# Kernel tuning notes

Hardware: AMD Instinct MI355X
Metric: run time of the kernel (lower is better)

## Reference

```python
import jax, jax.numpy as jnp
import numpy as np

N, E, H, B, L = 100000, 600000, 128, 512, 10


def setup_inputs() -> dict:
    key = jax.random.key(0)
    ks = jax.random.split(key, 16)
    def lin(k, fan_in, fan_out):
        return (jax.random.normal(k, (fan_in, fan_out), jnp.float32) / np.sqrt(fan_in)).astype(jnp.float32)
    inp = {
        'node_reps_0': jax.random.normal(ks[0], (N, H), jnp.float32),
        'node_reps_1': jax.random.normal(ks[1], (N, H), jnp.float32),
        'W1': lin(ks[2], 2 * H, 4 * H), 'b1': jnp.zeros((4 * H,), jnp.float32),
        'W2': lin(ks[3], 4 * H, 2 * H), 'b2': jnp.zeros((2 * H,), jnp.float32),
        'W3': lin(ks[4], 2 * H, H),     'b3': jnp.zeros((H,), jnp.float32),
        'W4': lin(ks[5], H, H),         'b4': jnp.zeros((H,), jnp.float32),
        'W5': lin(ks[6], H, L),         'b5': jnp.zeros((L,), jnp.float32),
        'edge_index': jax.random.randint(ks[7], (2, E), 0, N, jnp.int64 if jax.config.jax_enable_x64 else jnp.int32),
        'batch': jnp.sort(jax.random.randint(ks[8], (N,), 0, B)),
        'y': jax.random.randint(ks[9], (B,), 0, L),
    }
    return inp


def reference(node_reps_0, node_reps_1, W1, b1, W2, b2, W3, b3, W4, b4, W5, b5,
              edge_index, batch, y):
    # ava_node_reps = reps(full graph) - reps(occupied subgraph)
    reps = node_reps_0 - node_reps_1                      # [N, H]
    src, dst = edge_index[0], edge_index[1]               # [E]
    # gather endpoints, concat -> edge action rep MLP (ELU)
    a = jnp.concatenate([reps[src], reps[dst]], axis=1)   # [E, 2H]
    h = jax.nn.elu(a @ W1 + b1)                           # [E, 4H]
    h = jax.nn.elu(h @ W2 + b2)                           # [E, 2H]
    h = h @ W3 + b3                                       # [E, H]
    # edge action prob generator: h -> h -> num_labels
    logits = jax.nn.elu(h @ W4 + b4) @ W5 + b5            # [E, L]
    edge_batch = batch[src]                               # [E] graph id per edge
    target_y = y[edge_batch]                              # [E]
    scores = jnp.take_along_axis(logits, target_y[:, None], axis=1)[:, 0]  # [E]
    # segment-wise (per-graph) softmax over available edges
    seg_max = jax.ops.segment_max(scores, edge_batch, num_segments=B)
    ex = jnp.exp(scores - seg_max[edge_batch])
    seg_sum = jax.ops.segment_sum(ex, edge_batch, num_segments=B)
    probs = ex / seg_sum[edge_batch]                      # [E]
    # scatter_max: per-graph max prob and its (first) argmax edge index
    added_probs = jax.ops.segment_max(probs, edge_batch, num_segments=B)  # [B]
    idx = jnp.arange(E, dtype=edge_batch.dtype)
    cand = jnp.where(probs == added_probs[edge_batch], idx, E)
    added_actions = jax.ops.segment_min(cand, edge_batch, num_segments=B)  # [B]
    return probs, added_probs, added_actions
```

## Files before the change

kernel.cpp:

```cpp
#include <hip/hip_runtime.h>
#include <hip/hip_bf16.h>
#include <cmath>

#define NN 100000
#define EE 600000
#define BB 512
#define LL 10

typedef __attribute__((ext_vector_type(8))) short  bf16x8;
typedef __attribute__((ext_vector_type(4))) float  f32x4;
typedef unsigned int uint;
typedef unsigned short ushort;

__device__ __forceinline__ float elu_f(float x){ return x > 0.f ? x : __expf(x) - 1.f; }

__device__ __forceinline__ ushort bf16_rne(float f){
  uint u = __float_as_uint(f);
  return (ushort)((u + 0x7FFFu + ((u >> 16) & 1u)) >> 16);
}

__device__ __forceinline__ f32x4 MFMA(bf16x8 a, bf16x8 b, f32x4 c){
  return __builtin_amdgcn_mfma_f32_16x16x32_bf16(a, b, c, 0, 0, 0);
}

__device__ __forceinline__ unsigned enc_f(float f){
  unsigned u = __float_as_uint(f);
  return (u & 0x80000000u) ? ~u : (u | 0x80000000u);
}
__device__ __forceinline__ float dec_f(unsigned u){
  return (u & 0x80000000u) ? __uint_as_float(u ^ 0x80000000u) : __uint_as_float(~u);
}
#define ENC_NEG_INF 0x007FFFFFu

#define AROW 260

__global__ __launch_bounds__(256) void kReps(const float* __restrict__ r0,
                                             const float* __restrict__ r1,
                                             ushort* __restrict__ repsF){
  int gid = blockIdx.x*256 + threadIdx.x;
  int n = gid >> 4, k8 = gid & 15;
  const float4* a = (const float4*)(r0 + (size_t)n*128 + k8*8);
  const float4* b = (const float4*)(r1 + (size_t)n*128 + k8*8);
  float4 x0 = a[0], x1 = a[1], y0 = b[0], y1 = b[1];
  float d[8] = {x0.x-y0.x, x0.y-y0.y, x0.z-y0.z, x0.w-y0.w,
                x1.x-y1.x, x1.y-y1.y, x1.z-y1.z, x1.w-y1.w};
  ushort hi[8], lo[8];
  #pragma unroll
  for (int j=0;j<8;++j){
    hi[j] = bf16_rne(d[j]);
    float fh = __uint_as_float(((uint)hi[j])<<16);
    lo[j] = bf16_rne(d[j] - fh);
  }
  ushort* dh = repsF + (size_t)n*256 + k8*8;
  ushort* dl = dh + 128;
  #pragma unroll
  for (int j=0;j<8;++j){ dh[j] = hi[j]; dl[j] = lo[j]; }
}

__global__ __launch_bounds__(256) void kPrepW(const float* __restrict__ W, int N,
                                              int KT, int NT, ushort* __restrict__ dst){
  int gid = blockIdx.x*256 + threadIdx.x;
  int total = KT*NT*64;
  if (gid >= total) return;
  int l = gid & 63, tile = gid >> 6;
  int kt = tile / NT, nt = tile % NT;
  int kbase = kt*32 + (l>>4)*8;
  int n = nt*16 + (l&15);
  int partStride = KT*NT*512;
  int base = tile*512 + l*8;
  #pragma unroll
  for (int j=0;j<8;++j){
    float f = W[(size_t)(kbase+j)*N + n];
    ushort h = bf16_rne(f);
    float fh = __uint_as_float(((uint)h)<<16);
    dst[base + j] = h;
    dst[partStride + base + j] = bf16_rne(f - fh);
  }
}

template<int NTILES>
__device__ __forceinline__ void xposeN(ushort* sT, const f32x4* Cg,
                                       const float* __restrict__ biasPtr,
                                       bool doElu, int l){
  const int quad = l >> 4, r16 = l & 15;
  uint* ldsu = (uint*)sT;
  #pragma unroll
  for (int i = 0; i < NTILES; ++i){
    float bv = biasPtr[i*16 + r16];
    #pragma unroll
    for (int mtl = 0; mtl < 2; ++mtl){
      f32x4 v = Cg[i*2 + mtl];
      ushort hi[4], lo[4];
      #pragma unroll
      for (int r = 0; r < 4; ++r){
        float f = v[r] + bv;
        if (doElu) f = elu_f(f);
        hi[r] = bf16_rne(f);
        float fh = __uint_as_float(((uint)hi[r]) << 16);
        lo[r] = bf16_rne(f - fh);
      }
      uint v01h = (uint)hi[0] | ((uint)hi[1]<<16);
      uint v23h = (uint)hi[2] | ((uint)hi[3]<<16);
      uint v01l = (uint)lo[0] | ((uint)lo[1]<<16);
      uint v23l = (uint)lo[2] | ((uint)lo[3]<<16);
      uint t01h = __shfl_xor(v01h,1), t23h = __shfl_xor(v23h,1);
      uint t01l = __shfl_xor(v01l,1), t23l = __shfl_xor(v23l,1);
      int c2 = (i*16 + (r16 & ~1)) >> 1;
      int m0 = mtl*16 + quad*4;
      if (!(l & 1)){
        ldsu[(m0+0)*34 + c2]        = (v01h & 0xFFFFu) | (t01h << 16);
        ldsu[(m0+1)*34 + c2]        = (v01h >> 16) | (t01h & 0xFFFF0000u);
        ldsu[1088 + (m0+0)*34 + c2] = (v01l & 0xFFFFu) | (t01l << 16);
        ldsu[1088 + (m0+1)*34 + c2] = (v01l >> 16) | (t01l & 0xFFFF0000u);
      } else {
        ldsu[(m0+2)*34 + c2]        = (t23h & 0xFFFFu) | (v23h << 16);
        ldsu[(m0+3)*34 + c2]        = (t23h >> 16) | (v23h & 0xFFFF0000u);
        ldsu[1088 + (m0+2)*34 + c2] = (t23l & 0xFFFFu) | (v23l << 16);
        ldsu[1088 + (m0+3)*34 + c2] = (t23l >> 16) | (v23l & 0xFFFF0000u);
      }
    }
  }
}

__device__ __forceinline__ bf16x8 readA(const ushort* region, int part, int m, int colBase){
  union { uint2 u[2]; bf16x8 v; } cvt;
  const ushort* p = region + part*2176 + m*68 + colBase;
  cvt.u[0] = *(const uint2*)p;
  cvt.u[1] = *(const uint2*)(p + 4);
  return cvt.v;
}

__device__ __forceinline__ bf16x8 loadA8(const ushort* p){
  union { uint2 u[2]; bf16x8 v; } cvt;
  cvt.u[0] = *(const uint2*)p;
  cvt.u[1] = *(const uint2*)(p + 4);
  return cvt.v;
}

__device__ __forceinline__ void produceSlice(int s, int w, int l, int quad, int r16,
    const ushort* sA,
    const ushort* __restrict__ W1F, const float* __restrict__ b1,
    ushort* buf){
  f32x4 C1[2];
  C1[0] = (f32x4)0.f; C1[1] = (f32x4)0.f;
  #pragma unroll
  for (int hk = 0; hk < 8; ++hk){
    const int rbase = (hk < 4) ? 0 : 32;
    const int ko = (hk & 3)*32 + quad*8;
    const ushort* r0p = sA + (rbase + r16)*AROW + ko;
    const ushort* r1p = sA + (rbase + 16 + r16)*AROW + ko;
    bf16x8 Ah0 = loadA8(r0p);
    bf16x8 Al0 = loadA8(r0p + 128);
    bf16x8 Ah1 = loadA8(r1p);
    bf16x8 Al1 = loadA8(r1p + 128);
    const bf16x8* WfH = (const bf16x8*)W1F + ((size_t)hk*32 + s*4 + w)*64 + l;
    const bf16x8* WfL = WfH + 8*32*64;
    bf16x8 Bh = WfH[0], Bl = WfL[0];
    C1[0] = MFMA(Ah0, Bh, C1[0]); C1[1] = MFMA(Ah1, Bh, C1[1]);
    C1[0] = MFMA(Ah0, Bl, C1[0]); C1[1] = MFMA(Ah1, Bl, C1[1]);
    C1[0] = MFMA(Al0, Bh, C1[0]); C1[1] = MFMA(Al1, Bh, C1[1]);
  }
  xposeN<1>(buf + w*16, C1, b1 + s*64 + w*16, true, l);
}

__device__ __forceinline__ void consumeSlice(int s, int w, int l, int quad, int r16,
    const ushort* buf, const ushort* __restrict__ W2F, f32x4 (&C2q)[8]){
  #pragma unroll
  for (int j2 = 0; j2 < 2; ++j2){
    int colBase = j2*32 + quad*8;
    bf16x8 Ah[2], Al[2];
    #pragma unroll
    for (int mtl = 0; mtl < 2; ++mtl){
      int m = mtl*16 + r16;
      Ah[mtl] = readA(buf, 0, m, colBase);
      Al[mtl] = readA(buf, 1, m, colBase);
    }
    const int kt = s*2 + j2;
    const bf16x8* WfH = (const bf16x8*)W2F + ((size_t)kt*16 + w*4)*64 + l;
    const bf16x8* WfL = WfH + 16*16*64;
    #pragma unroll
    for (int j = 0; j < 4; ++j){
      bf16x8 Bh = WfH[j*64], Bl = WfL[j*64];
      f32x4 c0 = C2q[j*2], c1 = C2q[j*2+1];
      c0 = MFMA(Ah[0], Bh, c0); c1 = MFMA(Ah[1], Bh, c1);
      c0 = MFMA(Ah[0], Bl, c0); c1 = MFMA(Ah[1], Bl, c1);
      c0 = MFMA(Al[0], Bh, c0); c1 = MFMA(Al[1], Bh, c1);
      C2q[j*2] = c0; C2q[j*2+1] = c1;
    }
  }
}

__global__ __launch_bounds__(256, 4) void kMLP(
    const ushort* __restrict__ repsF,
    const ushort* __restrict__ W1F, const ushort* __restrict__ W2F,
    const ushort* __restrict__ W3F, const ushort* __restrict__ W4F,
    const float* __restrict__ b1, const float* __restrict__ b2,
    const float* __restrict__ b3, const float* __restrict__ b4,
    const float* __restrict__ W5, const float* __restrict__ b5,
    const int* __restrict__ edge_index, const int* __restrict__ batch,
    const int* __restrict__ y,
    float* __restrict__ scores, int* __restrict__ ebatch)
{
  __shared__ __align__(16) ushort sReg01[2*4352];
  __shared__ __align__(16) ushort sA[64*AROW];
  __shared__ int sTy[32];
  __shared__ int sNode[64];
  __shared__ float sRed[4][32];

  const int tid = threadIdx.x;
  const int w = tid >> 6;
  const int l = tid & 63;
  const int quad = l >> 4, r16 = l & 15;
  const int e0 = blockIdx.x * 32;

  if (tid < 32){
    int s = edge_index[e0 + tid];
    int d = edge_index[EE + e0 + tid];
    sNode[tid] = s;
    sNode[32 + tid] = d;
    int eb = batch[s];
    ebatch[e0 + tid] = eb;
    sTy[tid] = y[eb];
  }
  __syncthreads();

  #pragma unroll
  for (int k = 0; k < 8; ++k){
    int c = tid + k*256;
    int row = c >> 5, col = c & 31;
    const ushort* src = repsF + (size_t)sNode[row]*256 + col*8;
    uint4 v = *(const uint4*)src;
    ushort* dst = sA + row*AROW + col*8;
    *(uint2*)dst        = make_uint2(v.x, v.y);
    *(uint2*)(dst + 4)  = make_uint2(v.z, v.w);
  }
  __syncthreads();

  f32x4 C2q[8];
  #pragma unroll
  for (int i=0;i<8;++i) C2q[i] = (f32x4)0.f;

  produceSlice(0, w, l, quad, r16, sA, W1F, b1, sReg01);
  __syncthreads();
  #pragma unroll 1
  for (int s = 0; s < 8; ++s){
    if (s < 7)
      produceSlice(s+1, w, l, quad, r16, sA, W1F, b1, sReg01 + ((s+1)&1)*4352);
    consumeSlice(s, w, l, quad, r16, sReg01 + (s&1)*4352, W2F, C2q);
    __syncthreads();
  }

  ushort* regW = (w < 2) ? (sReg01 + w*4352) : (sA + (w-2)*4352);
  xposeN<4>(regW, C2q, b2 + w*64, true, l);
  __syncthreads();

  f32x4 C3q[4];
  #pragma unroll
  for (int i=0;i<4;++i) C3q[i] = (f32x4)0.f;
  #pragma unroll
  for (int kt = 0; kt < 8; ++kt){
    int rw = kt >> 1;
    const ushort* reg = (rw < 2) ? (sReg01 + rw*4352) : (sA + (rw-2)*4352);
    int colBase = (kt & 1)*32 + quad*8;
    bf16x8 Ah[2], Al[2];
    #pragma unroll
    for (int mtl = 0; mtl < 2; ++mtl){
      int m = mtl*16 + r16;
      Ah[mtl] = readA(reg, 0, m, colBase);
      Al[mtl] = readA(reg, 1, m, colBase);
    }
    const bf16x8* WfH = (const bf16x8*)W3F + ((size_t)kt*8 + w*2)*64 + l;
    const bf16x8* WfL = WfH + 8*8*64;
    #pragma unroll
    for (int j = 0; j < 2; ++j){
      bf16x8 Bh = WfH[j*64], Bl = WfL[j*64];
      f32x4 c0 = C3q[j*2], c1 = C3q[j*2+1];
      c0 = MFMA(Ah[0], Bh, c0); c1 = MFMA(Ah[1], Bh, c1);
      c0 = MFMA(Ah[0], Bl, c0); c1 = MFMA(Ah[1], Bl, c1);
      c0 = MFMA(Al[0], Bh, c0); c1 = MFMA(Al[1], Bh, c1);
      C3q[j*2] = c0; C3q[j*2+1] = c1;
    }
  }
  __syncthreads();

  xposeN<2>(sReg01 + (w>>1)*4352 + (w&1)*32, C3q, b3 + w*32, false, l);
  __syncthreads();

  f32x4 C4q[4];
  #pragma unroll
  for (int i=0;i<4;++i) C4q[i] = (f32x4)0.f;
  #pragma unroll
  for (int kt = 0; kt < 4; ++kt){
    const ushort* reg = sReg01 + (kt>>1)*4352;
    int colBase = (kt & 1)*32 + quad*8;
    bf16x8 Ah[2], Al[2];
    #pragma unroll
    for (int mtl = 0; mtl < 2; ++mtl){
      int m = mtl*16 + r16;
      Ah[mtl] = readA(reg, 0, m, colBase);
      Al[mtl] = readA(reg, 1, m, colBase);
    }
    const bf16x8* WfH = (const bf16x8*)W4F + ((size_t)kt*8 + w*2)*64 + l;
    const bf16x8* WfL = WfH + 4*8*64;
    #pragma unroll
    for (int j = 0; j < 2; ++j){
      bf16x8 Bh = WfH[j*64], Bl = WfL[j*64];
      f32x4 c0 = C4q[j*2], c1 = C4q[j*2+1];
      c0 = MFMA(Ah[0], Bh, c0); c1 = MFMA(Ah[1], Bh, c1);
      c0 = MFMA(Ah[0], Bl, c0); c1 = MFMA(Ah[1], Bl, c1);
      c0 = MFMA(Al[0], Bh, c0); c1 = MFMA(Al[1], Bh, c1);
      C4q[j*2] = c0; C4q[j*2+1] = c1;
    }
  }

  int tvals[2][4];
  #pragma unroll
  for (int mtl=0;mtl<2;++mtl)
    #pragma unroll
    for (int r=0;r<4;++r) tvals[mtl][r] = sTy[mtl*16 + quad*4 + r];

  float p[2][4] = {{0.f,0.f,0.f,0.f},{0.f,0.f,0.f,0.f}};
  #pragma unroll
  for (int j = 0; j < 2; ++j){
    int n4 = (w*2 + j)*16 + r16;
    float bv = b4[n4];
    const float* w5r = W5 + n4*LL;
    #pragma unroll
    for (int mtl = 0; mtl < 2; ++mtl){
      f32x4 c = C4q[j*2+mtl];
      #pragma unroll
      for (int r=0;r<4;++r)
        p[mtl][r] += elu_f(c[r] + bv) * w5r[tvals[mtl][r]];
    }
  }
  #pragma unroll
  for (int d = 8; d >= 1; d >>= 1){
    #pragma unroll
    for (int mtl=0;mtl<2;++mtl)
      #pragma unroll
      for (int r=0;r<4;++r)
        p[mtl][r] += __shfl_down(p[mtl][r], d, 16);
  }
  if (r16 == 0){
    #pragma unroll
    for (int mtl=0;mtl<2;++mtl)
      #pragma unroll
      for (int r=0;r<4;++r){
        int m = mtl*16 + quad*4 + r;
        sRed[w][m] = p[mtl][r];
      }
  }
  __syncthreads();
  if (tid < 32){
    float s = sRed[0][tid] + sRed[1][tid] + sRed[2][tid] + sRed[3][tid];
    scores[e0 + tid] = s + b5[sTy[tid]];
  }
}

__global__ void kInitSeg(unsigned* segmax, float* segsum, unsigned* gmax, int* gact){
  int b = blockIdx.x*blockDim.x + threadIdx.x;
  if (b < BB){ segmax[b] = ENC_NEG_INF; segsum[b] = 0.f; gmax[b] = ENC_NEG_INF; gact[b] = 0x7FFFFFFF; }
}

__global__ __launch_bounds__(256) void kSegMax(const float* __restrict__ scores,
                                               const int* __restrict__ eb,
                                               unsigned* __restrict__ segmax){
  __shared__ unsigned l[BB];
  for (int b = threadIdx.x; b < BB; b += 256) l[b] = 0u;
  __syncthreads();
  for (int e = blockIdx.x*256 + threadIdx.x; e < EE; e += gridDim.x*256)
    atomicMax(&l[eb[e]], enc_f(scores[e]));
  __syncthreads();
  for (int b = threadIdx.x; b < BB; b += 256)
    if (l[b]) atomicMax(&segmax[b], l[b]);
}

__global__ __launch_bounds__(256) void kExpSum(const float* __restrict__ scores,
                                               const int* __restrict__ eb,
                                               const unsigned* __restrict__ segmax,
                                               float* __restrict__ segsum,
                                               float* __restrict__ outprobs){
  __shared__ float l[BB];
  for (int b = threadIdx.x; b < BB; b += 256) l[b] = 0.f;
  __syncthreads();
  for (int e = blockIdx.x*256 + threadIdx.x; e < EE; e += gridDim.x*256){
    int b = eb[e];
    float ex = expf(scores[e] - dec_f(segmax[b]));
    outprobs[e] = ex;
    atomicAdd(&l[b], ex);
  }
  __syncthreads();
  for (int b = threadIdx.x; b < BB; b += 256)
    if (l[b] != 0.f) atomicAdd(&segsum[b], l[b]);
}

__global__ __launch_bounds__(256) void kProbMax(float* __restrict__ outprobs,
                                                const int* __restrict__ eb,
                                                const float* __restrict__ segsum,
                                                unsigned* __restrict__ gmax){
  __shared__ unsigned l[BB];
  for (int b = threadIdx.x; b < BB; b += 256) l[b] = 0u;
  __syncthreads();
  for (int e = blockIdx.x*256 + threadIdx.x; e < EE; e += gridDim.x*256){
    int b = eb[e];
    float p = outprobs[e] / segsum[b];
    outprobs[e] = p;
    atomicMax(&l[b], enc_f(p));
  }
  __syncthreads();
  for (int b = threadIdx.x; b < BB; b += 256)
    if (l[b]) atomicMax(&gmax[b], l[b]);
}

__global__ __launch_bounds__(256) void kArgMin(const float* __restrict__ outprobs,
                                               const int* __restrict__ eb,
                                               const unsigned* __restrict__ gmax,
                                               int* __restrict__ gact){
  __shared__ int l[BB];
  for (int b = threadIdx.x; b < BB; b += 256) l[b] = 0x7FFFFFFF;
  __syncthreads();
  for (int e = blockIdx.x*256 + threadIdx.x; e < EE; e += gridDim.x*256){
    int b = eb[e];
    if (enc_f(outprobs[e]) == gmax[b]) atomicMin(&l[b], e);
  }
  __syncthreads();
  for (int b = threadIdx.x; b < BB; b += 256)
    if (l[b] != 0x7FFFFFFF) atomicMin(&gact[b], l[b]);
}

__global__ void kFinal(const unsigned* __restrict__ gmax, const int* __restrict__ gact,
                       float* __restrict__ out){
  int b = threadIdx.x;
  if (b < BB){
    out[EE + b]      = dec_f(gmax[b]);
    out[EE + BB + b] = (float)gact[b];
  }
}

extern "C" void kernel_launch(void* const* d_in, const int* in_sizes, int n_in,
                              void* d_out, int out_size, void* d_ws, size_t ws_size,
                              hipStream_t stream){
  const float* r0 = (const float*)d_in[0];
  const float* r1 = (const float*)d_in[1];
  const float* W1 = (const float*)d_in[2];
  const float* b1 = (const float*)d_in[3];
  const float* W2 = (const float*)d_in[4];
  const float* b2 = (const float*)d_in[5];
  const float* W3 = (const float*)d_in[6];
  const float* b3 = (const float*)d_in[7];
  const float* W4 = (const float*)d_in[8];
  const float* b4 = (const float*)d_in[9];
  const float* W5 = (const float*)d_in[10];
  const float* b5 = (const float*)d_in[11];
  const int* edge_index = (const int*)d_in[12];
  const int* batch = (const int*)d_in[13];
  const int* y = (const int*)d_in[14];
  float* out = (float*)d_out;

  char* ws = (char*)d_ws;
  size_t off = 0;
  float*    scores = (float*)(ws + off);    off += (size_t)EE*4;
  int*      ebatch = (int*)(ws + off);      off += (size_t)EE*4;
  unsigned* segmax = (unsigned*)(ws + off); off += BB*4;
  float*    segsum = (float*)(ws + off);    off += BB*4;
  unsigned* gmax   = (unsigned*)(ws + off); off += BB*4;
  int*      gact   = (int*)(ws + off);      off += BB*4;
  off = (off + 511) & ~(size_t)511;
  ushort* repsF = (ushort*)(ws + off);      off += (size_t)NN*256*2;
  ushort* W1F   = (ushort*)(ws + off);      off += (size_t)2*8*32*512*2;
  ushort* W2F   = (ushort*)(ws + off);      off += (size_t)2*16*16*512*2;
  ushort* W3F   = (ushort*)(ws + off);      off += (size_t)2*8*8*512*2;
  ushort* W4F   = (ushort*)(ws + off);      off += (size_t)2*4*8*512*2;

  kInitSeg<<<2, 256, 0, stream>>>(segmax, segsum, gmax, gact);
  kReps<<<(NN*16)/256, 256, 0, stream>>>(r0, r1, repsF);
  kPrepW<<<(8*32*64)/256, 256, 0, stream>>>(W1, 512, 8, 32, W1F);
  kPrepW<<<(16*16*64)/256, 256, 0, stream>>>(W2, 256, 16, 16, W2F);
  kPrepW<<<(8*8*64)/256, 256, 0, stream>>>(W3, 128, 8, 8, W3F);
  kPrepW<<<(4*8*64)/256, 256, 0, stream>>>(W4, 128, 4, 8, W4F);

  kMLP<<<EE/32, 256, 0, stream>>>(repsF, W1F, W2F, W3F, W4F,
                                  b1, b2, b3, b4, W5, b5,
                                  edge_index, batch, y, scores, ebatch);

  kSegMax <<<256, 256, 0, stream>>>(scores, ebatch, segmax);
  kExpSum <<<256, 256, 0, stream>>>(scores, ebatch, segmax, segsum, out);
  kProbMax<<<256, 256, 0, stream>>>(out, ebatch, segsum, gmax);
  kArgMin <<<256, 256, 0, stream>>>(out, ebatch, gmax, gact);
  kFinal  <<<1, 512, 0, stream>>>(gmax, gact, out);
}
```

Before: 1.430 ms.

## Split layer-1 gather into src/dst halves to shrink shared memory

Layer 1 now runs in two phases. The src-node rows are gathered into a half-size sA, and the first-half K contributions for all 8 output slices go into register accumulators (C1s[8][2]). The dst rows are then loaded into the same buffer and the second half is finished inside the pipelined produce/consume loop. This cuts the shared-memory footprint so more blocks can reside per CU, but it holds 64 extra accumulator floats per thread and fully unrolls the loop, which risks register pressure or spills under the 256x4 launch bounds.

```diff
diff --git a/kernel.cpp b/kernel.cpp
--- a/kernel.cpp
+++ b/kernel.cpp
@@ -137,30 +137,26 @@
   return cvt.v;
 }
 
-__device__ __forceinline__ void produceSlice(int s, int w, int l, int quad, int r16,
-    const ushort* sA,
-    const ushort* __restrict__ W1F, const float* __restrict__ b1,
-    ushort* buf){
-  f32x4 C1[2];
-  C1[0] = (f32x4)0.f; C1[1] = (f32x4)0.f;
-  #pragma unroll
-  for (int hk = 0; hk < 8; ++hk){
-    const int rbase = (hk < 4) ? 0 : 32;
-    const int ko = (hk & 3)*32 + quad*8;
-    const ushort* r0p = sA + (rbase + r16)*AROW + ko;
-    const ushort* r1p = sA + (rbase + 16 + r16)*AROW + ko;
+__device__ __forceinline__ void produceHalf(int sl, int w, int l, int quad, int r16,
+    const ushort* sA, int hkBase,
+    const ushort* __restrict__ W1F, f32x4 (&C1)[2]){
+  #pragma unroll
+  for (int hh = 0; hh < 4; ++hh){
+    const int hk = hkBase + hh;
+    const int ko = hh*32 + quad*8;
+    const ushort* r0p = sA + r16*AROW + ko;
+    const ushort* r1p = sA + (16 + r16)*AROW + ko;
     bf16x8 Ah0 = loadA8(r0p);
     bf16x8 Al0 = loadA8(r0p + 128);
     bf16x8 Ah1 = loadA8(r1p);
     bf16x8 Al1 = loadA8(r1p + 128);
-    const bf16x8* WfH = (const bf16x8*)W1F + ((size_t)hk*32 + s*4 + w)*64 + l;
+    const bf16x8* WfH = (const bf16x8*)W1F + ((size_t)hk*32 + sl*4 + w)*64 + l;
     const bf16x8* WfL = WfH + 8*32*64;
     bf16x8 Bh = WfH[0], Bl = WfL[0];
     C1[0] = MFMA(Ah0, Bh, C1[0]); C1[1] = MFMA(Ah1, Bh, C1[1]);
     C1[0] = MFMA(Ah0, Bl, C1[0]); C1[1] = MFMA(Ah1, Bl, C1[1]);
     C1[0] = MFMA(Al0, Bh, C1[0]); C1[1] = MFMA(Al1, Bh, C1[1]);
   }
-  xposeN<1>(buf + w*16, C1, b1 + s*64 + w*16, true, l);
 }
 
 __device__ __forceinline__ void consumeSlice(int s, int w, int l, int quad, int r16,
@@ -202,7 +198,7 @@
     float* __restrict__ scores, int* __restrict__ ebatch)
 {
   __shared__ __align__(16) ushort sReg01[2*4352];
-  __shared__ __align__(16) ushort sA[64*AROW];
+  __shared__ __align__(16) ushort sA[2*4352];
   __shared__ int sTy[32];
   __shared__ int sNode[64];
   __shared__ float sRed[4][32];
@@ -225,7 +221,7 @@
   __syncthreads();
 
   #pragma unroll
-  for (int k = 0; k < 8; ++k){
+  for (int k = 0; k < 4; ++k){
     int c = tid + k*256;
     int row = c >> 5, col = c & 31;
     const ushort* src = repsF + (size_t)sNode[row]*256 + col*8;
@@ -236,19 +232,44 @@
   }
   __syncthreads();
 
+  f32x4 C1s[8][2];
+  #pragma unroll
+  for (int s=0;s<8;++s){ C1s[s][0] = (f32x4)0.f; C1s[s][1] = (f32x4)0.f; }
+  #pragma unroll
+  for (int s = 0; s < 8; ++s)
+    produceHalf(s, w, l, quad, r16, sA, 0, W1F, C1s[s]);
+
+  __syncthreads();
+
+  #pragma unroll
+  for (int k = 0; k < 4; ++k){
+    int c = tid + k*256;
+    int row = c >> 5, col = c & 31;
+    const ushort* src = repsF + (size_t)sNode[32 + row]*256 + col*8;
+    uint4 v = *(const uint4*)src;
+    ushort* dst = sA + row*AROW + col*8;
+    *(uint2*)dst        = make_uint2(v.x, v.y);
+    *(uint2*)(dst + 4)  = make_uint2(v.z, v.w);
+  }
+  __syncthreads();
+
   f32x4 C2q[8];
   #pragma unroll
   for (int i=0;i<8;++i) C2q[i] = (f32x4)0.f;
 
-  produceSlice(0, w, l, quad, r16, sA, W1F, b1, sReg01);
-  __syncthreads();
-  #pragma unroll 1
-  for (int s = 0; s < 8; ++s){
-    if (s < 7)
-      produceSlice(s+1, w, l, quad, r16, sA, W1F, b1, sReg01 + ((s+1)&1)*4352);
+  produceHalf(0, w, l, quad, r16, sA, 4, W1F, C1s[0]);
+  xposeN<1>(sReg01 + w*16, C1s[0], b1 + w*16, true, l);
+  __syncthreads();
+  #pragma unroll
+  for (int s = 0; s < 7; ++s){
+    produceHalf(s+1, w, l, quad, r16, sA, 4, W1F, C1s[s+1]);
+    xposeN<1>(sReg01 + ((s+1)&1)*4352 + w*16, C1s[s+1],
+              b1 + (s+1)*64 + w*16, true, l);
     consumeSlice(s, w, l, quad, r16, sReg01 + (s&1)*4352, W2F, C2q);
     __syncthreads();
   }
+  consumeSlice(7, w, l, quad, r16, sReg01 + 4352, W2F, C2q);
+  __syncthreads();
 
   ushort* regW = (w < 2) ? (sReg01 + w*4352) : (sA + (w-2)*4352);
   xposeN<4>(regW, C2q, b2 + w*64, true, l);
```

After: 1.666 ms. 16.5% more time.

## Fuse prob-max and argmin into one packed 64-bit atomicMin pass; relax MLP occupancy

Applied to the files above, without the earlier changes.

Merges the per-graph probability max and first-argmax kernels into a single pass. It packs the inverted encoded probability and the edge index into one 64-bit key reduced with atomicMin, which removes one full pass over the edges and one launch. It also lowers kMLP's launch_bounds minimum blocks per SM from 4 to 3, giving the compiler more registers at the cost of occupancy, and peels the last consume iteration out of the slice loop. The 64-bit shared and global atomics may be slower than 32-bit ones.

```diff
diff --git a/kernel.cpp b/kernel.cpp
--- a/kernel.cpp
+++ b/kernel.cpp
@@ -11,6 +11,7 @@
 typedef __attribute__((ext_vector_type(4))) float  f32x4;
 typedef unsigned int uint;
 typedef unsigned short ushort;
+typedef unsigned long long u64;
 
 __device__ __forceinline__ float elu_f(float x){ return x > 0.f ? x : __expf(x) - 1.f; }
 
@@ -190,7 +191,7 @@
   }
 }
 
-__global__ __launch_bounds__(256, 4) void kMLP(
+__global__ __launch_bounds__(256, 3) void kMLP(
     const ushort* __restrict__ repsF,
     const ushort* __restrict__ W1F, const ushort* __restrict__ W2F,
     const ushort* __restrict__ W3F, const ushort* __restrict__ W4F,
@@ -243,12 +244,13 @@
   produceSlice(0, w, l, quad, r16, sA, W1F, b1, sReg01);
   __syncthreads();
   #pragma unroll 1
-  for (int s = 0; s < 8; ++s){
-    if (s < 7)
-      produceSlice(s+1, w, l, quad, r16, sA, W1F, b1, sReg01 + ((s+1)&1)*4352);
+  for (int s = 0; s < 7; ++s){
+    produceSlice(s+1, w, l, quad, r16, sA, W1F, b1, sReg01 + ((s+1)&1)*4352);
     consumeSlice(s, w, l, quad, r16, sReg01 + (s&1)*4352, W2F, C2q);
     __syncthreads();
   }
+  consumeSlice(7, w, l, quad, r16, sReg01 + 4352, W2F, C2q);
+  __syncthreads();
 
   ushort* regW = (w < 2) ? (sReg01 + w*4352) : (sA + (w-2)*4352);
   xposeN<4>(regW, C2q, b2 + w*64, true, l);
@@ -357,9 +359,9 @@
   }
 }
 
-__global__ void kInitSeg(unsigned* segmax, float* segsum, unsigned* gmax, int* gact){
+__global__ void kInitSeg(unsigned* segmax, float* segsum, u64* gkey){
   int b = blockIdx.x*blockDim.x + threadIdx.x;
-  if (b < BB){ segmax[b] = ENC_NEG_INF; segsum[b] = 0.f; gmax[b] = ENC_NEG_INF; gact[b] = 0x7FFFFFFF; }
+  if (b < BB){ segmax[b] = ENC_NEG_INF; segsum[b] = 0.f; gkey[b] = ~0ull; }
 }
 
 __global__ __launch_bounds__(256) void kSegMax(const float* __restrict__ scores,
@@ -394,46 +396,32 @@
     if (l[b] != 0.f) atomicAdd(&segsum[b], l[b]);
 }
 
-__global__ __launch_bounds__(256) void kProbMax(float* __restrict__ outprobs,
-                                                const int* __restrict__ eb,
-                                                const float* __restrict__ segsum,
-                                                unsigned* __restrict__ gmax){
-  __shared__ unsigned l[BB];
-  for (int b = threadIdx.x; b < BB; b += 256) l[b] = 0u;
+__global__ __launch_bounds__(256) void kMaxArg(float* __restrict__ outprobs,
+                                               const int* __restrict__ eb,
+                                               const float* __restrict__ segsum,
+                                               u64* __restrict__ gkey){
+  __shared__ u64 l[BB];
+  for (int b = threadIdx.x; b < BB; b += 256) l[b] = ~0ull;
   __syncthreads();
   for (int e = blockIdx.x*256 + threadIdx.x; e < EE; e += gridDim.x*256){
     int b = eb[e];
     float p = outprobs[e] / segsum[b];
     outprobs[e] = p;
-    atomicMax(&l[b], enc_f(p));
+    u64 key = ((u64)(~enc_f(p)) << 32) | (unsigned)e;
+    atomicMin(&l[b], key);
   }
   __syncthreads();
   for (int b = threadIdx.x; b < BB; b += 256)
-    if (l[b]) atomicMax(&gmax[b], l[b]);
-}
-
-__global__ __launch_bounds__(256) void kArgMin(const float* __restrict__ outprobs,
-                                               const int* __restrict__ eb,
-                                               const unsigned* __restrict__ gmax,
-                                               int* __restrict__ gact){
-  __shared__ int l[BB];
-  for (int b = threadIdx.x; b < BB; b += 256) l[b] = 0x7FFFFFFF;
-  __syncthreads();
-  for (int e = blockIdx.x*256 + threadIdx.x; e < EE; e += gridDim.x*256){
-    int b = eb[e];
-    if (enc_f(outprobs[e]) == gmax[b]) atomicMin(&l[b], e);
-  }
-  __syncthreads();
-  for (int b = threadIdx.x; b < BB; b += 256)
-    if (l[b] != 0x7FFFFFFF) atomicMin(&gact[b], l[b]);
-}
-
-__global__ void kFinal(const unsigned* __restrict__ gmax, const int* __restrict__ gact,
-                       float* __restrict__ out){
+    if (l[b] != ~0ull) atomicMin(&gkey[b], l[b]);
+}
+
+__global__ void kFinal(const u64* __restrict__ gkey, float* __restrict__ out){
   int b = threadIdx.x;
   if (b < BB){
-    out[EE + b]      = dec_f(gmax[b]);
-    out[EE + BB + b] = (float)gact[b];
+    u64 k = gkey[b];
+    unsigned enc = ~(unsigned)(k >> 32);
+    out[EE + b]      = dec_f(enc);
+    out[EE + BB + b] = (float)(unsigned)(k & 0xFFFFFFFFu);
   }
 }
 
@@ -463,8 +451,8 @@
   int*      ebatch = (int*)(ws + off);      off += (size_t)EE*4;
   unsigned* segmax = (unsigned*)(ws + off); off += BB*4;
   float*    segsum = (float*)(ws + off);    off += BB*4;
-  unsigned* gmax   = (unsigned*)(ws + off); off += BB*4;
-  int*      gact   = (int*)(ws + off);      off += BB*4;
+  off = (off + 7) & ~(size_t)7;
+  u64*      gkey   = (u64*)(ws + off);      off += BB*8;
   off = (off + 511) & ~(size_t)511;
   ushort* repsF = (ushort*)(ws + off);      off += (size_t)NN*256*2;
   ushort* W1F   = (ushort*)(ws + off);      off += (size_t)2*8*32*512*2;
@@ -472,7 +460,7 @@
   ushort* W3F   = (ushort*)(ws + off);      off += (size_t)2*8*8*512*2;
   ushort* W4F   = (ushort*)(ws + off);      off += (size_t)2*4*8*512*2;
 
-  kInitSeg<<<2, 256, 0, stream>>>(segmax, segsum, gmax, gact);
+  kInitSeg<<<2, 256, 0, stream>>>(segmax, segsum, gkey);
   kReps<<<(NN*16)/256, 256, 0, stream>>>(r0, r1, repsF);
   kPrepW<<<(8*32*64)/256, 256, 0, stream>>>(W1, 512, 8, 32, W1F);
   kPrepW<<<(16*16*64)/256, 256, 0, stream>>>(W2, 256, 16, 16, W2F);
@@ -483,9 +471,8 @@
                                   b1, b2, b3, b4, W5, b5,
                                   edge_index, batch, y, scores, ebatch);
 
-  kSegMax <<<256, 256, 0, stream>>>(scores, ebatch, segmax);
-  kExpSum <<<256, 256, 0, stream>>>(scores, ebatch, segmax, segsum, out);
-  kProbMax<<<256, 256, 0, stream>>>(out, ebatch, segsum, gmax);
-  kArgMin <<<256, 256, 0, stream>>>(out, ebatch, gmax, gact);
-  kFinal  <<<1, 512, 0, stream>>>(gmax, gact, out);
-}
+  kSegMax<<<256, 256, 0, stream>>>(scores, ebatch, segmax);
+  kExpSum<<<256, 256, 0, stream>>>(scores, ebatch, segmax, segsum, out);
+  kMaxArg<<<256, 256, 0, stream>>>(out, ebatch, segsum, gkey);
+  kFinal <<<1, 512, 0, stream>>>(gkey, out);
+}
```

Result: no change. 1.418 ms (-0.9%).
